# Performance work log

Measured on AMD Instinct MI355X. Metric: run time of the kernel, lower is better.

The kernel has to match this reference:

```python
import jax, jax.numpy as jnp
import numpy as np

N_NODES = 50000
N_EDGES = 800000
IN_DIM = 128
NUM_HEADS = 8
OUT_DIM = 16


def setup_inputs() -> dict:
    key = jax.random.key(0)
    ks = jax.random.split(key, 12)
    s = 1.0 / np.sqrt(IN_DIM)
    return {
        "h": jax.random.normal(ks[0], (N_NODES, IN_DIM), jnp.float32),
        "e": jax.random.normal(ks[1], (N_EDGES, IN_DIM), jnp.float32),
        "src": jax.random.randint(ks[2], (N_EDGES,), 0, N_NODES, jnp.int32),
        "dst": jax.random.randint(ks[3], (N_EDGES,), 0, N_NODES, jnp.int32),
        "Wq": jax.random.normal(ks[4], (IN_DIM, NUM_HEADS * OUT_DIM), jnp.float32) * s,
        "bq": jax.random.normal(ks[5], (NUM_HEADS * OUT_DIM,), jnp.float32) * s,
        "Wk": jax.random.normal(ks[6], (IN_DIM, NUM_HEADS * OUT_DIM), jnp.float32) * s,
        "bk": jax.random.normal(ks[7], (NUM_HEADS * OUT_DIM,), jnp.float32) * s,
        "We": jax.random.normal(ks[8], (IN_DIM, NUM_HEADS * OUT_DIM), jnp.float32) * s,
        "be": jax.random.normal(ks[9], (NUM_HEADS * OUT_DIM,), jnp.float32) * s,
        "Wv": jax.random.normal(ks[10], (IN_DIM, NUM_HEADS * OUT_DIM), jnp.float32) * s,
        "bv": jax.random.normal(ks[11], (NUM_HEADS * OUT_DIM,), jnp.float32) * s,
    }


def reference(h, e, src, dst, Wq, bq, Wk, bk, We, be, Wv, bv):
    N = h.shape[0]
    H, D = NUM_HEADS, OUT_DIM
    Q = (h @ Wq + bq).reshape(N, H, D)
    K = (h @ Wk + bk).reshape(N, H, D)
    V = (h @ Wv + bv).reshape(N, H, D)
    # Edge projection E is computed in the original forward but unused in the score.
    E_proj = (e @ We + be).reshape(-1, H, D)
    del E_proj
    # edge-wise gather + dot-product score: [E, H]
    score = jnp.einsum("ehd,ehd->eh", K[src], Q[dst]) / np.sqrt(D)
    # graph softmax numerator: exp of clamped score, [E, H, 1]
    s = jnp.exp(jnp.clip(score, -5.0, 5.0))[..., None]
    # scatter-sum weighted V and score sums per destination node
    wV = jax.ops.segment_sum(V[src] * s, dst, num_segments=N)  # [N, H, D]
    z = jax.ops.segment_sum(s, dst, num_segments=N)            # [N, H, 1]
    return wV / (z + 1e-6)
```

## Files before the change

### kernel.cpp

```cpp
#include <hip/hip_runtime.h>

#define NN 50000
#define NE 800000

#define CAP 64

#define QKV_NPB 16
__global__ __launch_bounds__(64) void qkv_kernel(
    const float* __restrict__ h,
    const float* __restrict__ Wq, const float* __restrict__ bq,
    const float* __restrict__ Wk, const float* __restrict__ bk,
    const float* __restrict__ Wv, const float* __restrict__ bv,
    const int* __restrict__ src, const int* __restrict__ dst,
    int* __restrict__ counts, int* __restrict__ src_padded,
    float* __restrict__ Q, float* __restrict__ K, float* __restrict__ V)
{
    __shared__ float hs[QKV_NPB * 128];
    const int lane = threadIdx.x;
    const int n0 = blockIdx.x * QKV_NPB;

    {
        const int e0 = blockIdx.x * 256 + lane;
#pragma unroll
        for (int j = 0; j < 4; ++j) {
            const int e = e0 + j * 64;
            const int d = dst[e];
            const int r = atomicAdd(&counts[d], 1);
            if (r < CAP) src_padded[d * CAP + r] = src[e];
        }
    }

    {
        const float4* hsrc = (const float4*)(h + (size_t)n0 * 128);
#pragma unroll
        for (int t = 0; t < 8; ++t) {
            const int idx = lane + t * 64;
            ((float4*)hs)[idx] = hsrc[idx];
        }
    }
    __syncthreads();

    const int c0 = lane * 2;
    float acc[3][2][QKV_NPB];
#pragma unroll
    for (int m = 0; m < 3; ++m)
#pragma unroll
        for (int c = 0; c < 2; ++c)
#pragma unroll
            for (int n = 0; n < QKV_NPB; ++n) acc[m][c][n] = 0.f;

    for (int kk = 0; kk < 128; kk += 4) {
        float2 w[3][4];
#pragma unroll
        for (int j = 0; j < 4; ++j) {
            w[0][j] = *(const float2*)(Wq + (kk + j) * 128 + c0);
            w[1][j] = *(const float2*)(Wk + (kk + j) * 128 + c0);
            w[2][j] = *(const float2*)(Wv + (kk + j) * 128 + c0);
        }
#pragma unroll
        for (int n = 0; n < QKV_NPB; ++n) {
            const float4 hv = *((const float4*)hs + n * 32 + (kk >> 2));
            const float hx[4] = {hv.x, hv.y, hv.z, hv.w};
#pragma unroll
            for (int m = 0; m < 3; ++m)
#pragma unroll
                for (int j = 0; j < 4; ++j) {
                    acc[m][0][n] = fmaf(hx[j], w[m][j].x, acc[m][0][n]);
                    acc[m][1][n] = fmaf(hx[j], w[m][j].y, acc[m][1][n]);
                }
        }
    }

    const float2 b2[3] = { *(const float2*)(bq + c0),
                           *(const float2*)(bk + c0),
                           *(const float2*)(bv + c0) };
    float* const outp[3] = { Q, K, V };
#pragma unroll
    for (int m = 0; m < 3; ++m)
#pragma unroll
        for (int n = 0; n < QKV_NPB; ++n) {
            float2 o = make_float2(acc[m][0][n] + b2[m].x,
                                   acc[m][1][n] + b2[m].y);
            *(float2*)(outp[m] + (size_t)(n0 + n) * 128 + c0) = o;
        }
}

__global__ __launch_bounds__(256) void aggregate_kernel(
    const int* __restrict__ counts, const int* __restrict__ src_padded,
    const float* __restrict__ Q, const float* __restrict__ K,
    const float* __restrict__ V, float* __restrict__ out)
{
    const int n = (blockIdx.x * 256 + threadIdx.x) >> 6;
    if (n >= NN) return;
    const int lane = threadIdx.x & 63;
    const int hh = lane & 7;
    const int es = lane >> 3;

    const float4* Qv = (const float4*)Q + (size_t)n * 32 + hh * 4;
    const float4 q0 = Qv[0], q1 = Qv[1], q2 = Qv[2], q3 = Qv[3];

    float4 a0 = make_float4(0.f, 0.f, 0.f, 0.f);
    float4 a1 = a0, a2 = a0, a3 = a0;
    float z = 0.f;

    int cnt = counts[n];
    if (cnt > CAP) cnt = CAP;
    const int* __restrict__ bucket = src_padded + n * CAP;

    int j = es;
    for (; j + 8 < cnt; j += 16) {
        const int s0 = bucket[j];
        const int s1 = bucket[j + 8];
        const float4* K0 = (const float4*)K + (size_t)s0 * 32 + hh * 4;
        const float4* V0 = (const float4*)V + (size_t)s0 * 32 + hh * 4;
        const float4* K1 = (const float4*)K + (size_t)s1 * 32 + hh * 4;
        const float4* V1 = (const float4*)V + (size_t)s1 * 32 + hh * 4;
        const float4 ka0 = K0[0], ka1 = K0[1], ka2 = K0[2], ka3 = K0[3];
        const float4 va0 = V0[0], va1 = V0[1], va2 = V0[2], va3 = V0[3];
        const float4 kb0 = K1[0], kb1 = K1[1], kb2 = K1[2], kb3 = K1[3];
        const float4 vb0 = V1[0], vb1 = V1[1], vb2 = V1[2], vb3 = V1[3];

        float sc0 = ka0.x * q0.x + ka0.y * q0.y + ka0.z * q0.z + ka0.w * q0.w
                  + ka1.x * q1.x + ka1.y * q1.y + ka1.z * q1.z + ka1.w * q1.w
                  + ka2.x * q2.x + ka2.y * q2.y + ka2.z * q2.z + ka2.w * q2.w
                  + ka3.x * q3.x + ka3.y * q3.y + ka3.z * q3.z + ka3.w * q3.w;
        float sc1 = kb0.x * q0.x + kb0.y * q0.y + kb0.z * q0.z + kb0.w * q0.w
                  + kb1.x * q1.x + kb1.y * q1.y + kb1.z * q1.z + kb1.w * q1.w
                  + kb2.x * q2.x + kb2.y * q2.y + kb2.z * q2.z + kb2.w * q2.w
                  + kb3.x * q3.x + kb3.y * q3.y + kb3.z * q3.z + kb3.w * q3.w;
        sc0 = fminf(5.f, fmaxf(-5.f, sc0 * 0.25f));
        sc1 = fminf(5.f, fmaxf(-5.f, sc1 * 0.25f));
        const float sw0 = __expf(sc0);
        const float sw1 = __expf(sc1);
        z += sw0;
        a0.x = fmaf(sw0, va0.x, a0.x); a0.y = fmaf(sw0, va0.y, a0.y);
        a0.z = fmaf(sw0, va0.z, a0.z); a0.w = fmaf(sw0, va0.w, a0.w);
        a1.x = fmaf(sw0, va1.x, a1.x); a1.y = fmaf(sw0, va1.y, a1.y);
        a1.z = fmaf(sw0, va1.z, a1.z); a1.w = fmaf(sw0, va1.w, a1.w);
        a2.x = fmaf(sw0, va2.x, a2.x); a2.y = fmaf(sw0, va2.y, a2.y);
        a2.z = fmaf(sw0, va2.z, a2.z); a2.w = fmaf(sw0, va2.w, a2.w);
        a3.x = fmaf(sw0, va3.x, a3.x); a3.y = fmaf(sw0, va3.y, a3.y);
        a3.z = fmaf(sw0, va3.z, a3.z); a3.w = fmaf(sw0, va3.w, a3.w);
        z += sw1;
        a0.x = fmaf(sw1, vb0.x, a0.x); a0.y = fmaf(sw1, vb0.y, a0.y);
        a0.z = fmaf(sw1, vb0.z, a0.z); a0.w = fmaf(sw1, vb0.w, a0.w);
        a1.x = fmaf(sw1, vb1.x, a1.x); a1.y = fmaf(sw1, vb1.y, a1.y);
        a1.z = fmaf(sw1, vb1.z, a1.z); a1.w = fmaf(sw1, vb1.w, a1.w);
        a2.x = fmaf(sw1, vb2.x, a2.x); a2.y = fmaf(sw1, vb2.y, a2.y);
        a2.z = fmaf(sw1, vb2.z, a2.z); a2.w = fmaf(sw1, vb2.w, a2.w);
        a3.x = fmaf(sw1, vb3.x, a3.x); a3.y = fmaf(sw1, vb3.y, a3.y);
        a3.z = fmaf(sw1, vb3.z, a3.z); a3.w = fmaf(sw1, vb3.w, a3.w);
    }
    if (j < cnt) {
        const int s = bucket[j];
        const float4* Kv = (const float4*)K + (size_t)s * 32 + hh * 4;
        const float4* Vv = (const float4*)V + (size_t)s * 32 + hh * 4;
        const float4 k0 = Kv[0], k1 = Kv[1], k2 = Kv[2], k3 = Kv[3];
        const float4 v0 = Vv[0], v1 = Vv[1], v2 = Vv[2], v3 = Vv[3];
        float sc = k0.x * q0.x + k0.y * q0.y + k0.z * q0.z + k0.w * q0.w
                 + k1.x * q1.x + k1.y * q1.y + k1.z * q1.z + k1.w * q1.w
                 + k2.x * q2.x + k2.y * q2.y + k2.z * q2.z + k2.w * q2.w
                 + k3.x * q3.x + k3.y * q3.y + k3.z * q3.z + k3.w * q3.w;
        sc = fminf(5.f, fmaxf(-5.f, sc * 0.25f));
        const float sw = __expf(sc);
        z += sw;
        a0.x = fmaf(sw, v0.x, a0.x); a0.y = fmaf(sw, v0.y, a0.y);
        a0.z = fmaf(sw, v0.z, a0.z); a0.w = fmaf(sw, v0.w, a0.w);
        a1.x = fmaf(sw, v1.x, a1.x); a1.y = fmaf(sw, v1.y, a1.y);
        a1.z = fmaf(sw, v1.z, a1.z); a1.w = fmaf(sw, v1.w, a1.w);
        a2.x = fmaf(sw, v2.x, a2.x); a2.y = fmaf(sw, v2.y, a2.y);
        a2.z = fmaf(sw, v2.z, a2.z); a2.w = fmaf(sw, v2.w, a2.w);
        a3.x = fmaf(sw, v3.x, a3.x); a3.y = fmaf(sw, v3.y, a3.y);
        a3.z = fmaf(sw, v3.z, a3.z); a3.w = fmaf(sw, v3.w, a3.w);
    }

#pragma unroll
    for (int m = 8; m < 64; m <<= 1) {
        z    += __shfl_xor(z,    m, 64);
        a0.x += __shfl_xor(a0.x, m, 64); a0.y += __shfl_xor(a0.y, m, 64);
        a0.z += __shfl_xor(a0.z, m, 64); a0.w += __shfl_xor(a0.w, m, 64);
        a1.x += __shfl_xor(a1.x, m, 64); a1.y += __shfl_xor(a1.y, m, 64);
        a1.z += __shfl_xor(a1.z, m, 64); a1.w += __shfl_xor(a1.w, m, 64);
        a2.x += __shfl_xor(a2.x, m, 64); a2.y += __shfl_xor(a2.y, m, 64);
        a2.z += __shfl_xor(a2.z, m, 64); a2.w += __shfl_xor(a2.w, m, 64);
        a3.x += __shfl_xor(a3.x, m, 64); a3.y += __shfl_xor(a3.y, m, 64);
        a3.z += __shfl_xor(a3.z, m, 64); a3.w += __shfl_xor(a3.w, m, 64);
    }

    const float inv = 1.0f / (z + 1e-6f);
    if (es < 4) {
        float4 r = (es == 0) ? a0 : (es == 1) ? a1 : (es == 2) ? a2 : a3;
        r.x *= inv; r.y *= inv; r.z *= inv; r.w *= inv;
        ((float4*)out)[(size_t)n * 32 + hh * 4 + es] = r;
    }
}

extern "C" void kernel_launch(void* const* d_in, const int* in_sizes, int n_in,
                              void* d_out, int out_size, void* d_ws, size_t ws_size,
                              hipStream_t stream)
{
    const float* h  = (const float*)d_in[0];
    const int* src = (const int*)d_in[2];
    const int* dst = (const int*)d_in[3];
    const float* Wq = (const float*)d_in[4];
    const float* bq = (const float*)d_in[5];
    const float* Wk = (const float*)d_in[6];
    const float* bk = (const float*)d_in[7];
    const float* Wv = (const float*)d_in[10];
    const float* bv = (const float*)d_in[11];

    float* Q = (float*)d_ws;
    float* K = Q + (size_t)NN * 128;
    float* V = K + (size_t)NN * 128;
    int* counts     = (int*)(V + (size_t)NN * 128);
    int* src_padded = counts + NN;

    hipMemsetAsync(counts, 0, NN * sizeof(int), stream);

    qkv_kernel<<<NN / QKV_NPB, 64, 0, stream>>>(h, Wq, bq, Wk, bk, Wv, bv,
                                                src, dst, counts, src_padded,
                                                Q, K, V);
    aggregate_kernel<<<(NN * 64) / 256, 256, 0, stream>>>(counts, src_padded,
                                                          Q, K, V, (float*)d_out);
}
```

Baseline: 748.3 us.

## Interleave K and V rows and overlap edge-bucketing atomics with GEMM

K and V are stored interleaved per node in one KV buffer, so each gathered source node's K and V slices come from a single contiguous 1 KB row instead of two separate arrays. The edge-bucketing atomics are spread across four chunks of the projection loop, with each scattered src_padded store issued after a quarter of the FMA work, so atomic latency is hidden behind compute. This adds register pressure for the buffered dst/src values and the loop split may reduce unrolling.

Result: faster. 732.2 us (-2.2%).

```diff
diff --git a/kernel.cpp b/kernel.cpp
--- a/kernel.cpp
+++ b/kernel.cpp
@@ -13,20 +13,19 @@
     const float* __restrict__ Wv, const float* __restrict__ bv,
     const int* __restrict__ src, const int* __restrict__ dst,
     int* __restrict__ counts, int* __restrict__ src_padded,
-    float* __restrict__ Q, float* __restrict__ K, float* __restrict__ V)
+    float* __restrict__ Q, float* __restrict__ KV)
 {
     __shared__ float hs[QKV_NPB * 128];
     const int lane = threadIdx.x;
     const int n0 = blockIdx.x * QKV_NPB;
 
+    int dv[4], sv[4];
     {
         const int e0 = blockIdx.x * 256 + lane;
 #pragma unroll
         for (int j = 0; j < 4; ++j) {
-            const int e = e0 + j * 64;
-            const int d = dst[e];
-            const int r = atomicAdd(&counts[d], 1);
-            if (r < CAP) src_padded[d * CAP + r] = src[e];
+            dv[j] = dst[e0 + j * 64];
+            sv[j] = src[e0 + j * 64];
         }
     }
 
@@ -49,46 +48,54 @@
 #pragma unroll
             for (int n = 0; n < QKV_NPB; ++n) acc[m][c][n] = 0.f;
 
-    for (int kk = 0; kk < 128; kk += 4) {
-        float2 w[3][4];
-#pragma unroll
-        for (int j = 0; j < 4; ++j) {
-            w[0][j] = *(const float2*)(Wq + (kk + j) * 128 + c0);
-            w[1][j] = *(const float2*)(Wk + (kk + j) * 128 + c0);
-            w[2][j] = *(const float2*)(Wv + (kk + j) * 128 + c0);
+    for (int c = 0; c < 4; ++c) {
+        const int r = atomicAdd(&counts[dv[c]], 1);
+
+        const int k0 = c * 32;
+        for (int kk = k0; kk < k0 + 32; kk += 4) {
+            float2 w[3][4];
+#pragma unroll
+            for (int j = 0; j < 4; ++j) {
+                w[0][j] = *(const float2*)(Wq + (kk + j) * 128 + c0);
+                w[1][j] = *(const float2*)(Wk + (kk + j) * 128 + c0);
+                w[2][j] = *(const float2*)(Wv + (kk + j) * 128 + c0);
+            }
+#pragma unroll
+            for (int n = 0; n < QKV_NPB; ++n) {
+                const float4 hv = *((const float4*)hs + n * 32 + (kk >> 2));
+                const float hx[4] = {hv.x, hv.y, hv.z, hv.w};
+#pragma unroll
+                for (int m = 0; m < 3; ++m)
+#pragma unroll
+                    for (int j = 0; j < 4; ++j) {
+                        acc[m][0][n] = fmaf(hx[j], w[m][j].x, acc[m][0][n]);
+                        acc[m][1][n] = fmaf(hx[j], w[m][j].y, acc[m][1][n]);
+                    }
+            }
         }
-#pragma unroll
-        for (int n = 0; n < QKV_NPB; ++n) {
-            const float4 hv = *((const float4*)hs + n * 32 + (kk >> 2));
-            const float hx[4] = {hv.x, hv.y, hv.z, hv.w};
-#pragma unroll
-            for (int m = 0; m < 3; ++m)
-#pragma unroll
-                for (int j = 0; j < 4; ++j) {
-                    acc[m][0][n] = fmaf(hx[j], w[m][j].x, acc[m][0][n]);
-                    acc[m][1][n] = fmaf(hx[j], w[m][j].y, acc[m][1][n]);
-                }
-        }
+
+        if (r < CAP)
+            src_padded[(size_t)dv[c] * CAP + r] = sv[c];
     }
 
     const float2 b2[3] = { *(const float2*)(bq + c0),
                            *(const float2*)(bk + c0),
                            *(const float2*)(bv + c0) };
-    float* const outp[3] = { Q, K, V };
-#pragma unroll
-    for (int m = 0; m < 3; ++m)
-#pragma unroll
-        for (int n = 0; n < QKV_NPB; ++n) {
-            float2 o = make_float2(acc[m][0][n] + b2[m].x,
-                                   acc[m][1][n] + b2[m].y);
-            *(float2*)(outp[m] + (size_t)(n0 + n) * 128 + c0) = o;
-        }
+#pragma unroll
+    for (int n = 0; n < QKV_NPB; ++n) {
+        *(float2*)(Q  + (size_t)(n0 + n) * 128 + c0) =
+            make_float2(acc[0][0][n] + b2[0].x, acc[0][1][n] + b2[0].y);
+        *(float2*)(KV + (size_t)(n0 + n) * 256 + c0) =
+            make_float2(acc[1][0][n] + b2[1].x, acc[1][1][n] + b2[1].y);
+        *(float2*)(KV + (size_t)(n0 + n) * 256 + 128 + c0) =
+            make_float2(acc[2][0][n] + b2[2].x, acc[2][1][n] + b2[2].y);
+    }
 }
 
 __global__ __launch_bounds__(256) void aggregate_kernel(
     const int* __restrict__ counts, const int* __restrict__ src_padded,
-    const float* __restrict__ Q, const float* __restrict__ K,
-    const float* __restrict__ V, float* __restrict__ out)
+    const float* __restrict__ Q, const float* __restrict__ KV,
+    float* __restrict__ out)
 {
     const int n = (blockIdx.x * 256 + threadIdx.x) >> 6;
     if (n >= NN) return;
@@ -105,20 +112,19 @@
 
     int cnt = counts[n];
     if (cnt > CAP) cnt = CAP;
-    const int* __restrict__ bucket = src_padded + n * CAP;
+    const int* __restrict__ bucket = src_padded + (size_t)n * CAP;
+    const float4* __restrict__ KV4 = (const float4*)KV;
 
     int j = es;
     for (; j + 8 < cnt; j += 16) {
         const int s0 = bucket[j];
         const int s1 = bucket[j + 8];
-        const float4* K0 = (const float4*)K + (size_t)s0 * 32 + hh * 4;
-        const float4* V0 = (const float4*)V + (size_t)s0 * 32 + hh * 4;
-        const float4* K1 = (const float4*)K + (size_t)s1 * 32 + hh * 4;
-        const float4* V1 = (const float4*)V + (size_t)s1 * 32 + hh * 4;
-        const float4 ka0 = K0[0], ka1 = K0[1], ka2 = K0[2], ka3 = K0[3];
-        const float4 va0 = V0[0], va1 = V0[1], va2 = V0[2], va3 = V0[3];
-        const float4 kb0 = K1[0], kb1 = K1[1], kb2 = K1[2], kb3 = K1[3];
-        const float4 vb0 = V1[0], vb1 = V1[1], vb2 = V1[2], vb3 = V1[3];
+        const float4* B0 = KV4 + (size_t)s0 * 64 + hh * 4;
+        const float4* B1 = KV4 + (size_t)s1 * 64 + hh * 4;
+        const float4 ka0 = B0[0],  ka1 = B0[1],  ka2 = B0[2],  ka3 = B0[3];
+        const float4 va0 = B0[32], va1 = B0[33], va2 = B0[34], va3 = B0[35];
+        const float4 kb0 = B1[0],  kb1 = B1[1],  kb2 = B1[2],  kb3 = B1[3];
+        const float4 vb0 = B1[32], vb1 = B1[33], vb2 = B1[34], vb3 = B1[35];
 
         float sc0 = ka0.x * q0.x + ka0.y * q0.y + ka0.z * q0.z + ka0.w * q0.w
                   + ka1.x * q1.x + ka1.y * q1.y + ka1.z * q1.z + ka1.w * q1.w
@@ -153,10 +159,9 @@
     }
     if (j < cnt) {
         const int s = bucket[j];
-        const float4* Kv = (const float4*)K + (size_t)s * 32 + hh * 4;
-        const float4* Vv = (const float4*)V + (size_t)s * 32 + hh * 4;
-        const float4 k0 = Kv[0], k1 = Kv[1], k2 = Kv[2], k3 = Kv[3];
-        const float4 v0 = Vv[0], v1 = Vv[1], v2 = Vv[2], v3 = Vv[3];
+        const float4* B = KV4 + (size_t)s * 64 + hh * 4;
+        const float4 k0 = B[0],  k1 = B[1],  k2 = B[2],  k3 = B[3];
+        const float4 v0 = B[32], v1 = B[33], v2 = B[34], v3 = B[35];
         float sc = k0.x * q0.x + k0.y * q0.y + k0.z * q0.z + k0.w * q0.w
                  + k1.x * q1.x + k1.y * q1.y + k1.z * q1.z + k1.w * q1.w
                  + k2.x * q2.x + k2.y * q2.y + k2.z * q2.z + k2.w * q2.w
@@ -209,17 +214,16 @@
     const float* Wv = (const float*)d_in[10];
     const float* bv = (const float*)d_in[11];
 
-    float* Q = (float*)d_ws;
-    float* K = Q + (size_t)NN * 128;
-    float* V = K + (size_t)NN * 128;
-    int* counts     = (int*)(V + (size_t)NN * 128);
+    float* Q  = (float*)d_ws;
+    float* KV = Q + (size_t)NN * 128;
+    int* counts     = (int*)(KV + (size_t)NN * 256);
     int* src_padded = counts + NN;
 
     hipMemsetAsync(counts, 0, NN * sizeof(int), stream);
 
     qkv_kernel<<<NN / QKV_NPB, 64, 0, stream>>>(h, Wq, bq, Wk, bk, Wv, bv,
                                                 src, dst, counts, src_padded,
-                                                Q, K, V);
+                                                Q, KV);
     aggregate_kernel<<<(NN * 64) / 256, 256, 0, stream>>>(counts, src_padded,
-                                                          Q, K, V, (float*)d_out);
+                                                          Q, KV, (float*)d_out);
 }
```
